# Kernel optimization log

Hardware: AMD Instinct MI355X
Metric: run time of the kernel (lower is better)

## Reference

```python
import jax, jax.numpy as jnp
import numpy as np

# Complete K-ary forest: B trees, depth D levels, BFS node numbering per tree.
B, K, D = 64, 4, 6
V, L = 600, 256
N_PER = (K ** D - 1) // (K - 1)   # 1365 nodes per tree
N = B * N_PER                      # 87360 total nodes


def _schedule():
    """Per-(depth, sibling_index) groups, mirroring the torch decode_train loop
    for a complete K-ary forest. Returns list of (d, s, node_idx, parent_idx)."""
    starts = [(K ** d - 1) // (K - 1) for d in range(D)]  # level offsets within a tree
    tree_off = np.arange(B)[:, None] * N_PER
    groups = []
    for d in range(D):
        for s in (range(1) if d == 0 else range(K)):
            if d == 0:
                p = np.arange(1)                      # root
                par = None
            else:
                p = np.arange(K ** (d - 1)) * K + s   # positions with sib_pos == s
                par = (tree_off + starts[d - 1] + (p // K)[None, :]).reshape(-1)
            idx = (tree_off + starts[d] + p[None, :]).reshape(-1)
            groups.append((d, s, jnp.asarray(idx),
                           None if par is None else jnp.asarray(par)))
    return groups

GROUPS = _schedule()


def _lstm(gx, h, c, W_hh, b_ih, b_hh):
    # torch LSTMCell, gate order i, f, g, o; gx = x @ W_ih^T precomputed.
    gates = gx + b_ih + h @ W_hh.T + b_hh
    i, f, g, o = jnp.split(gates, 4, axis=1)
    c_new = jax.nn.sigmoid(f) * c + jax.nn.sigmoid(i) * jnp.tanh(g)
    return jax.nn.sigmoid(o) * jnp.tanh(c_new), c_new


def setup_inputs() -> dict:
    key = jax.random.key(0)
    ks = jax.random.split(key, 20)
    w = lambda k, shape, s=0.05: jax.random.normal(k, shape, dtype=jnp.float32) * s
    return {
        'z': w(ks[0], (B, L), 1.0),
        'features': jax.random.randint(ks[1], (N,), 0, V),
        'W_ih_p': w(ks[2], (4 * L, V)), 'W_hh_p': w(ks[3], (4 * L, L)),
        'b_ih_p': w(ks[4], (4 * L,)), 'b_hh_p': w(ks[5], (4 * L,)),
        'W_ih_s': w(ks[6], (4 * L, V)), 'W_hh_s': w(ks[7], (4 * L, L)),
        'b_ih_s': w(ks[8], (4 * L,)), 'b_hh_s': w(ks[9], (4 * L,)),
        'U_parent': w(ks[10], (L, L)), 'U_sibling': w(ks[11], (L, L)),
        'W_label': w(ks[12], (V, L)), 'b_label': w(ks[13], (V,)),
        'W_depth': w(ks[14], (1, L)), 'b_depth': w(ks[15], (1,)),
        'W_width': w(ks[16], (1, L)), 'b_width': w(ks[17], (1,)),
        'w_off_p': w(ks[18], (1, 1), 1.0), 'w_off_s': w(ks[19], (1, 1), 1.0),
    }


def reference(z, features, W_ih_p, W_hh_p, b_ih_p, b_hh_p,
              W_ih_s, W_hh_s, b_ih_s, b_hh_s, U_parent, U_sibling,
              W_label, b_label, W_depth, b_depth, W_width, b_width,
              w_off_p, w_off_s):
    h_p = jnp.zeros((N, L), jnp.float32)
    c_p = jnp.zeros((N, L), jnp.float32)
    h_s = jnp.zeros((N, L), jnp.float32)
    c_s = jnp.zeros((N, L), jnp.float32)
    pred_labels = jnp.zeros((N, V), jnp.float32)
    pred_is_parent = jnp.zeros((N,), jnp.float32)
    pred_has_sib = jnp.zeros((N,), jnp.float32)

    for d, s, idx, pidx in GROUPS:
        G = idx.shape[0]
        if d == 0:
            h_par, c_par = z, jnp.zeros((B, L), jnp.float32)
        else:
            h_par, c_par = h_p[pidx], c_p[pidx]
        if s == 0:
            h_prev = jnp.zeros((G, L), jnp.float32)
            c_prev = jnp.zeros((G, L), jnp.float32)
        else:
            h_prev, c_prev = h_s[idx - 1], c_s[idx - 1]
        # group-constant teacher flags for a complete K-ary tree
        is_par = 1.0 if d < D - 1 else 0.0
        has_sib = 1.0 if (d > 0 and s < K - 1) else 0.0

        h_pred = jnp.tanh(h_par @ U_parent.T + h_prev @ U_sibling.T)
        logits = h_pred @ W_label.T + b_label
        p_par = jax.nn.sigmoid(h_pred @ W_depth.T + b_depth)[:, 0]
        p_sib = jax.nn.sigmoid(h_pred @ W_width.T + b_width)[:, 0]
        logp = jax.nn.log_softmax(
            logits + w_off_p[0, 0] * is_par + w_off_s[0, 0] * has_sib, axis=1)

        lab = features[idx]
        gx_p = jnp.take(W_ih_p, lab, axis=1).T  # one-hot @ W_ih^T as a gather
        gx_s = jnp.take(W_ih_s, lab, axis=1).T
        hp_new, cp_new = _lstm(gx_p, h_par, c_par, W_hh_p, b_ih_p, b_hh_p)
        hs_new, cs_new = _lstm(gx_s, h_prev, c_prev, W_hh_s, b_ih_s, b_hh_s)

        h_p = h_p.at[idx].set(hp_new)
        c_p = c_p.at[idx].set(cp_new)
        h_s = h_s.at[idx].set(hs_new)
        c_s = c_s.at[idx].set(cs_new)
        pred_labels = pred_labels.at[idx].set(logp)
        pred_is_parent = pred_is_parent.at[idx].set(p_par)
        pred_has_sib = pred_has_sib.at[idx].set(p_sib)

    # pack [N, V+2]: log-softmax labels, p(is_parent), p(has_sibling)
    return jnp.concatenate(
        [pred_labels, pred_is_parent[:, None], pred_has_sib[:, None]], axis=1)
```

## Files before the change

kernel.cpp:

```cpp
#include <hip/hip_runtime.h>


typedef unsigned short u16;
typedef short bf16x8 __attribute__((ext_vector_type(8)));
typedef float f32x4 __attribute__((ext_vector_type(4)));

#define NPER 1365
#define VDIM 600
#define VD2  602

__device__ __forceinline__ float b2f(u16 h) {
  union { unsigned u; float f; } v; v.u = ((unsigned)h) << 16; return v.f;
}
__device__ __forceinline__ u16 f2bf(float f) {
  union { float f; unsigned u; } v; v.f = f;
  unsigned r = v.u + 0x7fff + ((v.u >> 16) & 1);
  return (u16)(r >> 16);
}
__device__ __forceinline__ float fsigm(float x) {
  return __fdividef(1.f, 1.f + __expf(-x));
}
__device__ __forceinline__ float ftanh(float x) {
  float e = __expf(-2.f * fabsf(x));
  float r = __fdividef(1.f - e, 1.f + e);
  return x < 0.f ? -r : r;
}

__device__ __forceinline__ void ladder(int r, int& off, int& pcs, int& start) {
  if (r < 64)        { off = 0;    pcs = 0; start = 1;   }
  else if (r < 320)  { off = 64;   pcs = 2; start = 5;   }
  else if (r < 1344) { off = 320;  pcs = 4; start = 21;  }
  else if (r < 5440) { off = 1344; pcs = 6; start = 85;  }
  else               { off = 5440; pcs = 8; start = 341; }
}

__global__ void k_pack(
    const float* __restrict__ Upar, const float* __restrict__ Whhp,
    const float* __restrict__ Usib, const float* __restrict__ Whhs,
    const float* __restrict__ z, const float* __restrict__ Wihp,
    const float* __restrict__ Wihs, const float* __restrict__ Wlab,
    const float* __restrict__ Wd, const float* __restrict__ Ww,
    const float* __restrict__ blab, const float* __restrict__ bd,
    const float* __restrict__ bw, const float* __restrict__ bihp,
    const float* __restrict__ bhhp, const float* __restrict__ bihs,
    const float* __restrict__ bhhs,
    u16* __restrict__ UPWHHP, u16* __restrict__ USWHHS, u16* __restrict__ ZBF,
    u16* __restrict__ WIHPT, u16* __restrict__ WIHST, u16* __restrict__ WEXT,
    float* __restrict__ BE, float* __restrict__ BP, float* __restrict__ BS) {
  int i = blockIdx.x * 256 + threadIdx.x;
  if (i < 327680) {
    int r = i >> 8, c = i & 255;
    UPWHHP[i] = f2bf(r < 256 ? Upar[(r << 8) | c] : Whhp[((r - 256) << 8) | c]);
    return;
  }
  i -= 327680;
  if (i < 327680) {
    int r = i >> 8, c = i & 255;
    USWHHS[i] = f2bf(r < 256 ? Usib[(r << 8) | c] : Whhs[((r - 256) << 8) | c]);
    return;
  }
  i -= 327680;
  if (i < 16384) { ZBF[i] = f2bf(z[i]); return; }
  i -= 16384;
  if (i < 614400) {
    int r = i >> 10, c = i & 1023;
    WIHPT[i] = f2bf(Wihp[c * VDIM + r]); return;
  }
  i -= 614400;
  if (i < 614400) {
    int r = i >> 10, c = i & 1023;
    WIHST[i] = f2bf(Wihs[c * VDIM + r]); return;
  }
  i -= 614400;
  if (i < VD2 * 256) {
    int r = i >> 8, c = i & 255;
    float v = (r < VDIM) ? Wlab[r * 256 + c] : ((r == VDIM) ? Wd[c] : Ww[c]);
    WEXT[i] = f2bf(v); return;
  }
  i -= VD2 * 256;
  if (i < VD2) { BE[i] = (i < VDIM) ? blab[i] : ((i == VDIM) ? bd[0] : bw[0]); return; }
  i -= VD2;
  if (i < 1024) { BP[i] = bihp[i] + bhhp[i]; return; }
  i -= 1024;
  if (i < 1024) { BS[i] = bihs[i] + bhhs[i]; return; }
}

__global__ __launch_bounds__(256) void k_dual(
    const u16* __restrict__ A, const u16* __restrict__ B,
    u16* __restrict__ ppdst, int ppoff, float* __restrict__ uproj,
    u16* __restrict__ hroot, u16* __restrict__ gates, int M) {
  __shared__ __align__(16) u16 As[128 * 40];
  __shared__ __align__(16) u16 Bs[128 * 40];
  const int m0 = blockIdx.x * 128, n0 = blockIdx.y * 128;
  const int tid = threadIdx.x;
  const int wave = tid >> 6, lane = tid & 63;
  const int quad = lane >> 4, lr = lane & 15;
  const int wm = (wave >> 1) * 64, wn = (wave & 1) * 64;
  const int srow = tid >> 2;
  const int sch = (tid & 3) << 3;

  f32x4 acc[4][4] = {};
  for (int t = 0; t < 8; ++t) {
    const int kk = t * 32;
    bf16x8 a0 = *(const bf16x8*)(A + (size_t)(m0 + srow) * 256 + kk + sch);
    bf16x8 a1 = *(const bf16x8*)(A + (size_t)(m0 + srow + 64) * 256 + kk + sch);
    bf16x8 b0 = *(const bf16x8*)(B + (size_t)(n0 + srow) * 256 + kk + sch);
    bf16x8 b1 = *(const bf16x8*)(B + (size_t)(n0 + srow + 64) * 256 + kk + sch);
    __syncthreads();
    *(bf16x8*)&As[srow * 40 + sch] = a0;
    *(bf16x8*)&As[(srow + 64) * 40 + sch] = a1;
    *(bf16x8*)&Bs[srow * 40 + sch] = b0;
    *(bf16x8*)&Bs[(srow + 64) * 40 + sch] = b1;
    __syncthreads();
    bf16x8 af[4], bfr[4];
#pragma unroll
    for (int tm = 0; tm < 4; ++tm)
      af[tm] = *(const bf16x8*)&As[(wm + tm * 16 + lr) * 40 + quad * 8];
#pragma unroll
    for (int tn = 0; tn < 4; ++tn)
      bfr[tn] = *(const bf16x8*)&Bs[(wn + tn * 16 + lr) * 40 + quad * 8];
#pragma unroll
    for (int tm = 0; tm < 4; ++tm)
#pragma unroll
      for (int tn = 0; tn < 4; ++tn)
        acc[tm][tn] = __builtin_amdgcn_mfma_f32_16x16x32_bf16(
            af[tm], bfr[tn], acc[tm][tn], 0, 0, 0);
  }

  const bool isg = (n0 >= 256);
#pragma unroll
  for (int tn = 0; tn < 4; ++tn) {
    int col = n0 + wn + tn * 16 + lr;
#pragma unroll
    for (int tm = 0; tm < 4; ++tm) {
#pragma unroll
      for (int r = 0; r < 4; ++r) {
        int row = m0 + wm + tm * 16 + quad * 4 + r;
        if (row >= M) continue;
        float v = acc[tm][tn][r];
        if (isg) {
          gates[(size_t)row * 1024 + (col - 256)] = f2bf(v);
        } else if (hroot) {
          hroot[(size_t)row * NPER * 256 + col] = f2bf(ftanh(v));
        } else if (uproj) {
          uproj[(size_t)row * 256 + col] = v;
        } else {
          ppdst[(size_t)(ppoff + row) * 256 + col] = f2bf(v);
        }
      }
    }
  }
}


__global__ __launch_bounds__(256) void k_lstm_s0(
    const u16* __restrict__ wihT, const float* __restrict__ bias,
    const int* __restrict__ feat, u16* __restrict__ h, u16* __restrict__ c) {
  int r = blockIdx.x, u = threadIdx.x;
  int off, pcs, start; ladder(r, off, pcs, start);
  int lg = r - off;
  int t = lg >> pcs, j = lg & ((1 << pcs) - 1);
  int idx = t * NPER + start + 4 * j;
  int lab = feat[idx];
  const u16* wr = wihT + lab * 1024;
  float gi = b2f(wr[u])       + bias[u];
  float gg = b2f(wr[512 + u]) + bias[512 + u];
  float go = b2f(wr[768 + u]) + bias[768 + u];
  float cn = fsigm(gi) * ftanh(gg);
  float hn = fsigm(go) * ftanh(cn);
  h[(size_t)r * 256 + u] = f2bf(hn);
  c[(size_t)r * 256 + u] = f2bf(cn);
}

__global__ __launch_bounds__(256) void k_lstm_sibA(
    const u16* __restrict__ gates, const u16* __restrict__ wihT,
    const float* __restrict__ bias, const u16* __restrict__ c_in,
    const int* __restrict__ feat, u16* __restrict__ h, u16* __restrict__ c,
    int k) {
  int r = blockIdx.x, u = threadIdx.x;
  int off, pcs, start; ladder(r, off, pcs, start);
  int lg = r - off;
  int t = lg >> pcs, j = lg & ((1 << pcs) - 1);
  int idx = t * NPER + start + 4 * j + k;
  int lab = feat[idx];
  const u16* wr = wihT + lab * 1024;
  const u16* gr = gates + (size_t)r * 1024;
  float gi = b2f(wr[u])       + bias[u]       + b2f(gr[u]);
  float gf = b2f(wr[256 + u]) + bias[256 + u] + b2f(gr[256 + u]);
  float gg = b2f(wr[512 + u]) + bias[512 + u] + b2f(gr[512 + u]);
  float go = b2f(wr[768 + u]) + bias[768 + u] + b2f(gr[768 + u]);
  float cv = b2f(c_in[(size_t)r * 256 + u]);
  float cn = fsigm(gf) * cv + fsigm(gi) * ftanh(gg);
  float hn = fsigm(go) * ftanh(cn);
  h[(size_t)r * 256 + u] = f2bf(hn);
  c[(size_t)r * 256 + u] = f2bf(cn);
}

__global__ __launch_bounds__(256) void k_lstm_par(
    const u16* __restrict__ gates, const u16* __restrict__ wihT,
    const float* __restrict__ bias, const u16* __restrict__ c_in,
    const int* __restrict__ feat, u16* __restrict__ h, u16* __restrict__ c,
    int lsbits, int start) {
  int g = blockIdx.x, u = threadIdx.x;
  int t = g >> lsbits, p = g & ((1 << lsbits) - 1);
  int pr = lsbits ? ((t << (lsbits - 2)) | (p >> 2)) : g;
  int idx = t * NPER + start + p;
  int lab = feat[idx];
  const u16* wr = wihT + lab * 1024;
  const u16* gr = gates + (size_t)pr * 1024;
  float gi = b2f(wr[u])       + bias[u]       + b2f(gr[u]);
  float gf = b2f(wr[256 + u]) + bias[256 + u] + b2f(gr[256 + u]);
  float gg = b2f(wr[512 + u]) + bias[512 + u] + b2f(gr[512 + u]);
  float go = b2f(wr[768 + u]) + bias[768 + u] + b2f(gr[768 + u]);
  float cv = c_in ? b2f(c_in[(size_t)pr * 256 + u]) : 0.f;
  float cn = fsigm(gf) * cv + fsigm(gi) * ftanh(gg);
  float hn = fsigm(go) * ftanh(cn);
  h[(size_t)g * 256 + u] = f2bf(hn);
  c[(size_t)g * 256 + u] = f2bf(cn);
}

__global__ __launch_bounds__(256) void k_assemble(
    const u16* __restrict__ PPA, const float* __restrict__ U1,
    const float* __restrict__ U2, const float* __restrict__ U3,
    u16* __restrict__ HPRED) {
  int r = blockIdx.x, u = threadIdx.x;
  int off, pcs, start; ladder(r, off, pcs, start);
  int lg = r - off;
  int t = lg >> pcs, j = lg & ((1 << pcs) - 1);
  size_t base = ((size_t)(t * NPER + start + 4 * j)) * 256 + u;
  size_t ro = (size_t)r * 256 + u;
  float pp = b2f(PPA[ro]);
  HPRED[base]       = f2bf(ftanh(pp));
  HPRED[base + 256] = f2bf(ftanh(pp + U1[ro]));
  HPRED[base + 512] = f2bf(ftanh(pp + U2[ro]));
  HPRED[base + 768] = f2bf(ftanh(pp + U3[ro]));
}

__global__ __launch_bounds__(256, 2) void k_mm_tail(
    const u16* __restrict__ A, const u16* __restrict__ B,
    const float* __restrict__ bias, float* __restrict__ out) {
  __shared__ __align__(16) u16 As[32 * 264];
  __shared__ float smax[32][4], ssum[32][4], slz[32];
  const int m0 = blockIdx.x * 32;
  const int tid = threadIdx.x;
  const int wave = tid >> 6, lane = tid & 63;
  const int quad = lane >> 4, lr = lane & 15;
  const int c0 = wave * 160;

#pragma unroll
  for (int c = 0; c < 4; ++c) {
    int idx = c * 256 + tid;
    int row = idx >> 5, ch = (idx & 31) << 3;
    *(bf16x8*)&As[row * 264 + ch] =
        *(const bf16x8*)(A + (size_t)(m0 + row) * 256 + ch);
  }
  __syncthreads();

  f32x4 acc[2][10] = {};
#pragma unroll
  for (int t = 0; t < 8; ++t) {
    bf16x8 af[2], bfr[10];
#pragma unroll
    for (int tm = 0; tm < 2; ++tm)
      af[tm] = *(const bf16x8*)&As[(tm * 16 + lr) * 264 + t * 32 + quad * 8];
#pragma unroll
    for (int tn = 0; tn < 10; ++tn)
      bfr[tn] = *(const bf16x8*)(B + (size_t)(c0 + tn * 16 + lr) * 256 +
                                 t * 32 + quad * 8);
#pragma unroll
    for (int tm = 0; tm < 2; ++tm)
#pragma unroll
      for (int tn = 0; tn < 10; ++tn)
        acc[tm][tn] = __builtin_amdgcn_mfma_f32_16x16x32_bf16(
            af[tm], bfr[tn], acc[tm][tn], 0, 0, 0);
  }

  float bv[10]; bool val[10];
#pragma unroll
  for (int tn = 0; tn < 10; ++tn) {
    int col = c0 + tn * 16 + lr;
    val[tn] = (col < VDIM);
    bv[tn] = (col < VD2) ? bias[col] : 0.f;
  }

#pragma unroll
  for (int tm = 0; tm < 2; ++tm) {
#pragma unroll
    for (int r = 0; r < 4; ++r) {
      float mx = -1e30f;
#pragma unroll
      for (int tn = 0; tn < 10; ++tn)
        if (val[tn]) mx = fmaxf(mx, acc[tm][tn][r] + bv[tn]);
#pragma unroll
      for (int o = 1; o < 16; o <<= 1) mx = fmaxf(mx, __shfl_xor(mx, o, 64));
      if (lr == 0) smax[tm * 16 + quad * 4 + r][wave] = mx;
    }
  }
  __syncthreads();
#pragma unroll
  for (int tm = 0; tm < 2; ++tm) {
#pragma unroll
    for (int r = 0; r < 4; ++r) {
      int row = tm * 16 + quad * 4 + r;
      float fm = fmaxf(fmaxf(smax[row][0], smax[row][1]),
                       fmaxf(smax[row][2], smax[row][3]));
      float se = 0.f;
#pragma unroll
      for (int tn = 0; tn < 10; ++tn)
        if (val[tn]) se += __expf(acc[tm][tn][r] + bv[tn] - fm);
#pragma unroll
      for (int o = 1; o < 16; o <<= 1) se += __shfl_xor(se, o, 64);
      if (lr == 0) ssum[row][wave] = se;
    }
  }
  __syncthreads();
  if (tid < 32) {
    float fm = fmaxf(fmaxf(smax[tid][0], smax[tid][1]),
                     fmaxf(smax[tid][2], smax[tid][3]));
    slz[tid] = fm + __logf(ssum[tid][0] + ssum[tid][1] +
                           ssum[tid][2] + ssum[tid][3]);
  }
  __syncthreads();

#pragma unroll
  for (int tm = 0; tm < 2; ++tm) {
#pragma unroll
    for (int tn = 0; tn < 10; ++tn) {
      int col = c0 + tn * 16 + lr;
      if (col >= VD2) continue;
#pragma unroll
      for (int r = 0; r < 4; ++r) {
        int row = tm * 16 + quad * 4 + r;
        float v = acc[tm][tn][r] + bv[tn];
        out[(size_t)(m0 + row) * VD2 + col] =
            (col < VDIM) ? (v - slz[row]) : fsigm(v);
      }
    }
  }
}


extern "C" void kernel_launch(void* const* d_in, const int* in_sizes, int n_in,
                              void* d_out, int out_size, void* d_ws, size_t ws_size,
                              hipStream_t stream) {
  const float* z    = (const float*)d_in[0];
  const int*   feat = (const int*)d_in[1];
  const float* Wihp = (const float*)d_in[2];
  const float* Whhp = (const float*)d_in[3];
  const float* bihp = (const float*)d_in[4];
  const float* bhhp = (const float*)d_in[5];
  const float* Wihs = (const float*)d_in[6];
  const float* Whhs = (const float*)d_in[7];
  const float* bihs = (const float*)d_in[8];
  const float* bhhs = (const float*)d_in[9];
  const float* Upar = (const float*)d_in[10];
  const float* Usib = (const float*)d_in[11];
  const float* Wlab = (const float*)d_in[12];
  const float* blab = (const float*)d_in[13];
  const float* Wd   = (const float*)d_in[14];
  const float* bd   = (const float*)d_in[15];
  const float* Ww   = (const float*)d_in[16];
  const float* bw   = (const float*)d_in[17];
  float* out = (float*)d_out;

  char* w = (char*)d_ws;
  auto alloc = [&](size_t bytes) {
    char* p = w; w += (bytes + 255) & ~(size_t)255; return p;
  };
  u16*   UPWHHP = (u16*)alloc((size_t)1280 * 256 * 2);
  u16*   USWHHS = (u16*)alloc((size_t)1280 * 256 * 2);
  u16*   ZBF    = (u16*)alloc((size_t)128 * 256 * 2);
  u16*   WIHPT  = (u16*)alloc((size_t)VDIM * 1024 * 2);
  u16*   WIHST  = (u16*)alloc((size_t)VDIM * 1024 * 2);
  u16*   WEXT   = (u16*)alloc((size_t)640 * 256 * 2);
  float* BE     = (float*)alloc(VD2 * 4);
  float* BP     = (float*)alloc(1024 * 4);
  float* BS     = (float*)alloc(1024 * 4);
  const size_t CR = 21888;
  u16*   HSA[3], *CSA[3];
  for (int k = 0; k < 3; ++k) {
    HSA[k] = (u16*)alloc(CR * 256 * 2);
    CSA[k] = (u16*)alloc(CR * 256 * 2);
  }
  float* UPROJ[3];
  for (int k = 0; k < 3; ++k) UPROJ[k] = (float*)alloc(CR * 256 * 4);
  u16*   PPA   = (u16*)alloc(CR * 256 * 2);
  const size_t SB = (size_t)16384 * 256 * 2;
  u16* HP[2] = {(u16*)alloc(SB), (u16*)alloc(SB)};
  u16* CP[2] = {(u16*)alloc(SB), (u16*)alloc(SB)};
  u16*   GATES  = (u16*)alloc(CR * 1024 * 2);
  u16*   GATESP = (u16*)alloc((size_t)4096 * 1024 * 2);
  u16*   HPRED  = (u16*)alloc((size_t)87424 * 256 * 2);

  const int ppoff[6] = {0, 0, 64, 320, 1344, 5440};

  k_pack<<<8037, 256, 0, stream>>>(Upar, Whhp, Usib, Whhs, z, Wihp, Wihs,
                                   Wlab, Wd, Ww, blab, bd, bw, bihp, bhhp,
                                   bihs, bhhs, UPWHHP, USWHHS, ZBF, WIHPT,
                                   WIHST, WEXT, BE, BP, BS);
  k_lstm_s0<<<21824, 256, 0, stream>>>(WIHST, BS, feat, HSA[0], CSA[0]);

  k_dual<<<dim3(171, 10), 256, 0, stream>>>(HSA[0], USWHHS, nullptr, 0,
                                            UPROJ[0], nullptr, GATES, 21824);
  k_lstm_sibA<<<21824, 256, 0, stream>>>(GATES, WIHST, BS, CSA[0], feat,
                                         HSA[1], CSA[1], 1);
  k_dual<<<dim3(171, 10), 256, 0, stream>>>(HSA[1], USWHHS, nullptr, 0,
                                            UPROJ[1], nullptr, GATES, 21824);
  k_lstm_sibA<<<21824, 256, 0, stream>>>(GATES, WIHST, BS, CSA[1], feat,
                                         HSA[2], CSA[2], 2);
  k_dual<<<dim3(171, 2), 256, 0, stream>>>(HSA[2], USWHHS, nullptr, 0,
                                           UPROJ[2], nullptr, nullptr, 21824);

  k_dual<<<dim3(1, 10), 256, 0, stream>>>(ZBF, UPWHHP, nullptr, 0, nullptr,
                                          HPRED, GATESP, 64);
  k_lstm_par<<<64, 256, 0, stream>>>(GATESP, WIHPT, BP, nullptr, feat,
                                     HP[0], CP[0], 0, 0);
  const int starts[6] = {0, 1, 5, 21, 85, 341};
  int cur = 0;
  for (int d = 0; d < 4; ++d) {
    const int M = 64 << (2 * d);
    k_dual<<<dim3((M + 127) / 128, 10), 256, 0, stream>>>(
        HP[cur], UPWHHP, PPA, ppoff[d + 1], nullptr, nullptr, GATESP, M);
    k_lstm_par<<<64 << (2 * (d + 1)), 256, 0, stream>>>(
        GATESP, WIHPT, BP, CP[cur], feat, HP[1 - cur], CP[1 - cur],
        2 * (d + 1), starts[d + 1]);
    cur = 1 - cur;
  }
  k_dual<<<dim3(128, 2), 256, 0, stream>>>(HP[cur], UPWHHP, PPA, ppoff[5],
                                           nullptr, nullptr, nullptr, 16384);

  k_assemble<<<21824, 256, 0, stream>>>(PPA, UPROJ[0], UPROJ[1], UPROJ[2],
                                        HPRED);
  k_mm_tail<<<2730, 256, 0, stream>>>(HPRED, WEXT, BE, out);

  (void)in_sizes; (void)n_in; (void)out_size; (void)ws_size;
}
```

Baseline: 650.9 us.

## Co-schedule independent sibling and parent chains in fused launches, fold assemble into GEMM epilogue

Merges the independent sibling-chain and parent-chain kernels into combined launches that split work by block index. This cuts the launch count and lets small parent-level GEMMs and LSTMs overlap with the large sibling work. The assemble step for deeper levels moves into the parent GEMM epilogue, which shrinks the PPA buffer and removes a read/write pass. Output and UPROJ stores become nontemporal. Fused kernels pay for the largest shared-memory and register footprint of any branch, and the modes add some branching.

After: 863.2 us. 1.33x slower.

```diff
diff --git a/kernel.cpp b/kernel.cpp
--- a/kernel.cpp
+++ b/kernel.cpp
@@ -8,6 +8,11 @@
 #define NPER 1365
 #define VDIM 600
 #define VD2  602
+
+#define MODE_PPA   0
+#define MODE_UPROJ 1
+#define MODE_ROOT  2
+#define MODE_EPI   3
 
 __device__ __forceinline__ float b2f(u16 h) {
   union { unsigned u; float f; } v; v.u = ((unsigned)h) << 16; return v.f;
@@ -85,13 +90,16 @@
   if (i < 1024) { BS[i] = bihs[i] + bhhs[i]; return; }
 }
 
-__global__ __launch_bounds__(256) void k_dual(
-    const u16* __restrict__ A, const u16* __restrict__ B,
-    u16* __restrict__ ppdst, int ppoff, float* __restrict__ uproj,
-    u16* __restrict__ hroot, u16* __restrict__ gates, int M) {
-  __shared__ __align__(16) u16 As[128 * 40];
-  __shared__ __align__(16) u16 Bs[128 * 40];
-  const int m0 = blockIdx.x * 128, n0 = blockIdx.y * 128;
+__device__ __forceinline__ void dev_dual(
+    int tile, int nx, const u16* __restrict__ A, const u16* __restrict__ B,
+    int M, int mode, u16* __restrict__ ppa, int ppoff,
+    float* __restrict__ uproj, u16* __restrict__ gates,
+    u16* __restrict__ hpred, const float* __restrict__ U1,
+    const float* __restrict__ U2, const float* __restrict__ U3,
+    int lsb, int startd) {
+  static __shared__ __align__(16) u16 As[128 * 40];
+  static __shared__ __align__(16) u16 Bs[128 * 40];
+  const int m0 = (tile % nx) * 128, n0 = (tile / nx) * 128;
   const int tid = threadIdx.x;
   const int wave = tid >> 6, lane = tid & 63;
   const int quad = lane >> 4, lr = lane & 15;
@@ -140,12 +148,20 @@
         float v = acc[tm][tn][r];
         if (isg) {
           gates[(size_t)row * 1024 + (col - 256)] = f2bf(v);
-        } else if (hroot) {
-          hroot[(size_t)row * NPER * 256 + col] = f2bf(ftanh(v));
-        } else if (uproj) {
-          uproj[(size_t)row * 256 + col] = v;
+        } else if (mode == MODE_PPA) {
+          ppa[(size_t)(ppoff + row) * 256 + col] = f2bf(v);
+        } else if (mode == MODE_UPROJ) {
+          __builtin_nontemporal_store(v, &uproj[(size_t)row * 256 + col]);
+        } else if (mode == MODE_ROOT) {
+          hpred[(size_t)row * NPER * 256 + col] = f2bf(ftanh(v));
         } else {
-          ppdst[(size_t)(ppoff + row) * 256 + col] = f2bf(v);
+          int t2 = row >> lsb, j = row & ((1 << lsb) - 1);
+          size_t bb = ((size_t)(t2 * NPER + startd + 4 * j)) * 256 + col;
+          size_t ro = (size_t)(ppoff + row) * 256 + col;
+          hpred[bb]       = f2bf(ftanh(v));
+          hpred[bb + 256] = f2bf(ftanh(v + U1[ro]));
+          hpred[bb + 512] = f2bf(ftanh(v + U2[ro]));
+          hpred[bb + 768] = f2bf(ftanh(v + U3[ro]));
         }
       }
     }
@@ -153,15 +169,14 @@
 }
 
 
-__global__ __launch_bounds__(256) void k_lstm_s0(
-    const u16* __restrict__ wihT, const float* __restrict__ bias,
-    const int* __restrict__ feat, u16* __restrict__ h, u16* __restrict__ c) {
-  int r = blockIdx.x, u = threadIdx.x;
+__device__ __forceinline__ void dev_s0(int r, const u16* __restrict__ wihT,
+    const float* __restrict__ bias, const int* __restrict__ feat,
+    u16* __restrict__ h, u16* __restrict__ c) {
+  int u = threadIdx.x;
   int off, pcs, start; ladder(r, off, pcs, start);
   int lg = r - off;
   int t = lg >> pcs, j = lg & ((1 << pcs) - 1);
-  int idx = t * NPER + start + 4 * j;
-  int lab = feat[idx];
+  int lab = feat[t * NPER + start + 4 * j];
   const u16* wr = wihT + lab * 1024;
   float gi = b2f(wr[u])       + bias[u];
   float gg = b2f(wr[512 + u]) + bias[512 + u];
@@ -172,17 +187,15 @@
   c[(size_t)r * 256 + u] = f2bf(cn);
 }
 
-__global__ __launch_bounds__(256) void k_lstm_sibA(
+__device__ __forceinline__ void dev_lstm_sib(int r, int k,
     const u16* __restrict__ gates, const u16* __restrict__ wihT,
     const float* __restrict__ bias, const u16* __restrict__ c_in,
-    const int* __restrict__ feat, u16* __restrict__ h, u16* __restrict__ c,
-    int k) {
-  int r = blockIdx.x, u = threadIdx.x;
+    const int* __restrict__ feat, u16* __restrict__ h, u16* __restrict__ c) {
+  int u = threadIdx.x;
   int off, pcs, start; ladder(r, off, pcs, start);
   int lg = r - off;
   int t = lg >> pcs, j = lg & ((1 << pcs) - 1);
-  int idx = t * NPER + start + 4 * j + k;
-  int lab = feat[idx];
+  int lab = feat[t * NPER + start + 4 * j + k];
   const u16* wr = wihT + lab * 1024;
   const u16* gr = gates + (size_t)r * 1024;
   float gi = b2f(wr[u])       + bias[u]       + b2f(gr[u]);
@@ -196,16 +209,15 @@
   c[(size_t)r * 256 + u] = f2bf(cn);
 }
 
-__global__ __launch_bounds__(256) void k_lstm_par(
+__device__ __forceinline__ void dev_lstm_par(int g,
     const u16* __restrict__ gates, const u16* __restrict__ wihT,
     const float* __restrict__ bias, const u16* __restrict__ c_in,
     const int* __restrict__ feat, u16* __restrict__ h, u16* __restrict__ c,
     int lsbits, int start) {
-  int g = blockIdx.x, u = threadIdx.x;
+  int u = threadIdx.x;
   int t = g >> lsbits, p = g & ((1 << lsbits) - 1);
   int pr = lsbits ? ((t << (lsbits - 2)) | (p >> 2)) : g;
-  int idx = t * NPER + start + p;
-  int lab = feat[idx];
+  int lab = feat[t * NPER + start + p];
   const u16* wr = wihT + lab * 1024;
   const u16* gr = gates + (size_t)pr * 1024;
   float gi = b2f(wr[u])       + bias[u]       + b2f(gr[u]);
@@ -219,11 +231,11 @@
   c[(size_t)g * 256 + u] = f2bf(cn);
 }
 
-__global__ __launch_bounds__(256) void k_assemble(
+__device__ __forceinline__ void dev_assemble(int r,
     const u16* __restrict__ PPA, const float* __restrict__ U1,
     const float* __restrict__ U2, const float* __restrict__ U3,
     u16* __restrict__ HPRED) {
-  int r = blockIdx.x, u = threadIdx.x;
+  int u = threadIdx.x;
   int off, pcs, start; ladder(r, off, pcs, start);
   int lg = r - off;
   int t = lg >> pcs, j = lg & ((1 << pcs) - 1);
@@ -236,6 +248,72 @@
   HPRED[base + 768] = f2bf(ftanh(pp + U3[ro]));
 }
 
+
+__global__ __launch_bounds__(256) void k_s0_zdual(
+    const u16* WIHST, const float* BS, const int* feat, u16* h, u16* c,
+    const u16* ZBF, const u16* UPWHHP, u16* HPRED, u16* GATESP) {
+  int b = blockIdx.x;
+  if (b < 21824)
+    dev_s0(b, WIHST, BS, feat, h, c);
+  else
+    dev_dual(b - 21824, 1, ZBF, UPWHHP, 64, MODE_ROOT, nullptr, 0, nullptr,
+             GATESP, HPRED, nullptr, nullptr, nullptr, 0, 0);
+}
+
+__global__ __launch_bounds__(256) void k_sibdual_plstm(
+    int nSib, int nx, const u16* HSAin, const u16* USWHHS,
+    float* UPROJk, u16* GATES,
+    const u16* GATESP, const u16* WIHPT, const float* BP, const u16* CPin,
+    const int* feat, u16* HPout, u16* CPout, int lsbits, int startp) {
+  int b = blockIdx.x;
+  if (b < nSib)
+    dev_dual(b, nx, HSAin, USWHHS, 21824, MODE_UPROJ, nullptr, 0, UPROJk,
+             GATES, nullptr, nullptr, nullptr, nullptr, 0, 0);
+  else
+    dev_lstm_par(b - nSib, GATESP, WIHPT, BP, CPin, feat, HPout, CPout,
+                 lsbits, startp);
+}
+
+__global__ __launch_bounds__(256) void k_siblstm_pdual(
+    int kSib, const u16* GATES, const u16* WIHST, const float* BS,
+    const u16* CSAin, const int* feat, u16* HSAout, u16* CSAout,
+    int nx, const u16* HPin, const u16* UPWHHP, int Mpar,
+    u16* PPA, int ppoff, u16* GATESP) {
+  int b = blockIdx.x;
+  if (b < 21824)
+    dev_lstm_sib(b, kSib, GATES, WIHST, BS, CSAin, feat, HSAout, CSAout);
+  else
+    dev_dual(b - 21824, nx, HPin, UPWHHP, Mpar, MODE_PPA, PPA, ppoff, nullptr,
+             GATESP, nullptr, nullptr, nullptr, nullptr, 0, 0);
+}
+
+__global__ __launch_bounds__(256) void k_pdual_epi(
+    int nx, const u16* HPin, const u16* UPWHHP, int M, u16* GATESP,
+    u16* HPRED, const float* U1, const float* U2, const float* U3,
+    int ppoff, int lsb, int startd) {
+  dev_dual(blockIdx.x, nx, HPin, UPWHHP, M, MODE_EPI, nullptr, ppoff, nullptr,
+           GATESP, HPRED, U1, U2, U3, lsb, startd);
+}
+
+__global__ __launch_bounds__(256) void k_plstm_asm(
+    const u16* GATESP, const u16* WIHPT, const float* BP, const u16* CPin,
+    const int* feat, u16* HPout, u16* CPout,
+    const u16* PPA, const float* U1, const float* U2, const float* U3,
+    u16* HPRED) {
+  int b = blockIdx.x;
+  if (b < 4096)
+    dev_lstm_par(b, GATESP, WIHPT, BP, CPin, feat, HPout, CPout, 6, 21);
+  else
+    dev_assemble(b - 4096, PPA, U1, U2, U3, HPRED);
+}
+
+__global__ __launch_bounds__(256) void k_plstm(
+    const u16* GATESP, const u16* WIHPT, const float* BP, const u16* CPin,
+    const int* feat, u16* HPout, u16* CPout, int lsbits, int start) {
+  dev_lstm_par(blockIdx.x, GATESP, WIHPT, BP, CPin, feat, HPout, CPout,
+               lsbits, start);
+}
+
 __global__ __launch_bounds__(256, 2) void k_mm_tail(
     const u16* __restrict__ A, const u16* __restrict__ B,
     const float* __restrict__ bias, float* __restrict__ out) {
@@ -332,8 +410,8 @@
       for (int r = 0; r < 4; ++r) {
         int row = tm * 16 + quad * 4 + r;
         float v = acc[tm][tn][r] + bv[tn];
-        out[(size_t)(m0 + row) * VD2 + col] =
-            (col < VDIM) ? (v - slz[row]) : fsigm(v);
+        float o = (col < VDIM) ? (v - slz[row]) : fsigm(v);
+        __builtin_nontemporal_store(o, &out[(size_t)(m0 + row) * VD2 + col]);
       }
     }
   }
@@ -384,7 +462,7 @@
   }
   float* UPROJ[3];
   for (int k = 0; k < 3; ++k) UPROJ[k] = (float*)alloc(CR * 256 * 4);
-  u16*   PPA   = (u16*)alloc(CR * 256 * 2);
+  u16*   PPA   = (u16*)alloc((size_t)384 * 256 * 2);
   const size_t SB = (size_t)16384 * 256 * 2;
   u16* HP[2] = {(u16*)alloc(SB), (u16*)alloc(SB)};
   u16* CP[2] = {(u16*)alloc(SB), (u16*)alloc(SB)};
@@ -392,45 +470,41 @@
   u16*   GATESP = (u16*)alloc((size_t)4096 * 1024 * 2);
   u16*   HPRED  = (u16*)alloc((size_t)87424 * 256 * 2);
 
-  const int ppoff[6] = {0, 0, 64, 320, 1344, 5440};
-
   k_pack<<<8037, 256, 0, stream>>>(Upar, Whhp, Usib, Whhs, z, Wihp, Wihs,
                                    Wlab, Wd, Ww, blab, bd, bw, bihp, bhhp,
                                    bihs, bhhs, UPWHHP, USWHHS, ZBF, WIHPT,
                                    WIHST, WEXT, BE, BP, BS);
-  k_lstm_s0<<<21824, 256, 0, stream>>>(WIHST, BS, feat, HSA[0], CSA[0]);
-
-  k_dual<<<dim3(171, 10), 256, 0, stream>>>(HSA[0], USWHHS, nullptr, 0,
-                                            UPROJ[0], nullptr, GATES, 21824);
-  k_lstm_sibA<<<21824, 256, 0, stream>>>(GATES, WIHST, BS, CSA[0], feat,
-                                         HSA[1], CSA[1], 1);
-  k_dual<<<dim3(171, 10), 256, 0, stream>>>(HSA[1], USWHHS, nullptr, 0,
-                                            UPROJ[1], nullptr, GATES, 21824);
-  k_lstm_sibA<<<21824, 256, 0, stream>>>(GATES, WIHST, BS, CSA[1], feat,
-                                         HSA[2], CSA[2], 2);
-  k_dual<<<dim3(171, 2), 256, 0, stream>>>(HSA[2], USWHHS, nullptr, 0,
-                                           UPROJ[2], nullptr, nullptr, 21824);
-
-  k_dual<<<dim3(1, 10), 256, 0, stream>>>(ZBF, UPWHHP, nullptr, 0, nullptr,
-                                          HPRED, GATESP, 64);
-  k_lstm_par<<<64, 256, 0, stream>>>(GATESP, WIHPT, BP, nullptr, feat,
-                                     HP[0], CP[0], 0, 0);
-  const int starts[6] = {0, 1, 5, 21, 85, 341};
-  int cur = 0;
-  for (int d = 0; d < 4; ++d) {
-    const int M = 64 << (2 * d);
-    k_dual<<<dim3((M + 127) / 128, 10), 256, 0, stream>>>(
-        HP[cur], UPWHHP, PPA, ppoff[d + 1], nullptr, nullptr, GATESP, M);
-    k_lstm_par<<<64 << (2 * (d + 1)), 256, 0, stream>>>(
-        GATESP, WIHPT, BP, CP[cur], feat, HP[1 - cur], CP[1 - cur],
-        2 * (d + 1), starts[d + 1]);
-    cur = 1 - cur;
-  }
-  k_dual<<<dim3(128, 2), 256, 0, stream>>>(HP[cur], UPWHHP, PPA, ppoff[5],
-                                           nullptr, nullptr, nullptr, 16384);
-
-  k_assemble<<<21824, 256, 0, stream>>>(PPA, UPROJ[0], UPROJ[1], UPROJ[2],
-                                        HPRED);
+  k_s0_zdual<<<21834, 256, 0, stream>>>(WIHST, BS, feat, HSA[0], CSA[0],
+                                        ZBF, UPWHHP, HPRED, GATESP);
+  k_sibdual_plstm<<<1710 + 64, 256, 0, stream>>>(
+      1710, 171, HSA[0], USWHHS, UPROJ[0], GATES,
+      GATESP, WIHPT, BP, nullptr, feat, HP[0], CP[0], 0, 0);
+  k_siblstm_pdual<<<21824 + 10, 256, 0, stream>>>(
+      1, GATES, WIHST, BS, CSA[0], feat, HSA[1], CSA[1],
+      1, HP[0], UPWHHP, 64, PPA, 0, GATESP);
+  k_sibdual_plstm<<<1710 + 256, 256, 0, stream>>>(
+      1710, 171, HSA[1], USWHHS, UPROJ[1], GATES,
+      GATESP, WIHPT, BP, CP[0], feat, HP[1], CP[1], 2, 1);
+  k_siblstm_pdual<<<21824 + 20, 256, 0, stream>>>(
+      2, GATES, WIHST, BS, CSA[1], feat, HSA[2], CSA[2],
+      2, HP[1], UPWHHP, 256, PPA, 64, GATESP);
+  k_sibdual_plstm<<<342 + 1024, 256, 0, stream>>>(
+      342, 171, HSA[2], USWHHS, UPROJ[2], nullptr,
+      GATESP, WIHPT, BP, CP[1], feat, HP[0], CP[0], 4, 5);
+  k_pdual_epi<<<80, 256, 0, stream>>>(8, HP[0], UPWHHP, 1024, GATESP,
+                                      HPRED, UPROJ[0], UPROJ[1], UPROJ[2],
+                                      320, 4, 21);
+  k_plstm_asm<<<4096 + 320, 256, 0, stream>>>(
+      GATESP, WIHPT, BP, CP[0], feat, HP[1], CP[1],
+      PPA, UPROJ[0], UPROJ[1], UPROJ[2], HPRED);
+  k_pdual_epi<<<320, 256, 0, stream>>>(32, HP[1], UPWHHP, 4096, GATESP,
+                                       HPRED, UPROJ[0], UPROJ[1], UPROJ[2],
+                                       1344, 6, 85);
+  k_plstm<<<16384, 256, 0, stream>>>(GATESP, WIHPT, BP, CP[1], feat,
+                                     HP[0], CP[0], 8, 85);
+  k_pdual_epi<<<256, 256, 0, stream>>>(128, HP[0], UPWHHP, 16384, nullptr,
+                                       HPRED, UPROJ[0], UPROJ[1], UPROJ[2],
+                                       5440, 8, 341);
   k_mm_tail<<<2730, 256, 0, stream>>>(HPRED, WEXT, BE, out);
 
   (void)in_sizes; (void)n_in; (void)out_size; (void)ws_size;
```

## Co-schedule parent and sibling chains in merged launches and fuse assemble into tail

Applied to the files above, without the earlier changes.

The independent parent-LSTM and sibling-LSTM chains now share grids: their GEMM tiles are combined in one k_gg launch and their elementwise LSTM steps in one k_ll launch, cutting launch count and letting the small parent-level work overlap with the large sibling work. The k_assemble pass and the HPRED buffer are removed. The tail kernel now builds h_pred tiles on the fly from PPA and UPROJ with tanh, and the root rows come from a separate HROOT buffer. The tail tile also shrinks from 32 to 16 rows with a higher occupancy bound. The trade-off is that B weights are reloaded twice as often in the tail, and the tail's load path now has more divergent indexing.

Measured after the change: 727.2 us. +11.7%, slower.

```diff
diff --git a/kernel.cpp b/kernel.cpp
--- a/kernel.cpp
+++ b/kernel.cpp
@@ -8,6 +8,10 @@
 #define NPER 1365
 #define VDIM 600
 #define VD2  602
+
+#define MODE_PPA   0
+#define MODE_UPROJ 1
+#define MODE_ROOT  2
 
 __device__ __forceinline__ float b2f(u16 h) {
   union { unsigned u; float f; } v; v.u = ((unsigned)h) << 16; return v.f;
@@ -85,13 +89,14 @@
   if (i < 1024) { BS[i] = bihs[i] + bhhs[i]; return; }
 }
 
-__global__ __launch_bounds__(256) void k_dual(
-    const u16* __restrict__ A, const u16* __restrict__ B,
-    u16* __restrict__ ppdst, int ppoff, float* __restrict__ uproj,
-    u16* __restrict__ hroot, u16* __restrict__ gates, int M) {
-  __shared__ __align__(16) u16 As[128 * 40];
-  __shared__ __align__(16) u16 Bs[128 * 40];
-  const int m0 = blockIdx.x * 128, n0 = blockIdx.y * 128;
+__device__ __forceinline__ void dev_dual(
+    int tile, int nx, const u16* __restrict__ A, const u16* __restrict__ B,
+    int M, int mode, u16* __restrict__ ppa, int ppoff,
+    float* __restrict__ uproj, u16* __restrict__ gates,
+    u16* __restrict__ hroot) {
+  static __shared__ __align__(16) u16 As[128 * 40];
+  static __shared__ __align__(16) u16 Bs[128 * 40];
+  const int m0 = (tile % nx) * 128, n0 = (tile / nx) * 128;
   const int tid = threadIdx.x;
   const int wave = tid >> 6, lane = tid & 63;
   const int quad = lane >> 4, lr = lane & 15;
@@ -140,12 +145,12 @@
         float v = acc[tm][tn][r];
         if (isg) {
           gates[(size_t)row * 1024 + (col - 256)] = f2bf(v);
-        } else if (hroot) {
-          hroot[(size_t)row * NPER * 256 + col] = f2bf(ftanh(v));
-        } else if (uproj) {
+        } else if (mode == MODE_PPA) {
+          ppa[(size_t)(ppoff + row) * 256 + col] = f2bf(v);
+        } else if (mode == MODE_UPROJ) {
           uproj[(size_t)row * 256 + col] = v;
         } else {
-          ppdst[(size_t)(ppoff + row) * 256 + col] = f2bf(v);
+          hroot[(size_t)row * 256 + col] = f2bf(ftanh(v));
         }
       }
     }
@@ -153,15 +158,14 @@
 }
 
 
-__global__ __launch_bounds__(256) void k_lstm_s0(
-    const u16* __restrict__ wihT, const float* __restrict__ bias,
-    const int* __restrict__ feat, u16* __restrict__ h, u16* __restrict__ c) {
-  int r = blockIdx.x, u = threadIdx.x;
+__device__ __forceinline__ void dev_s0(int r, const u16* __restrict__ wihT,
+    const float* __restrict__ bias, const int* __restrict__ feat,
+    u16* __restrict__ h, u16* __restrict__ c) {
+  int u = threadIdx.x;
   int off, pcs, start; ladder(r, off, pcs, start);
   int lg = r - off;
   int t = lg >> pcs, j = lg & ((1 << pcs) - 1);
-  int idx = t * NPER + start + 4 * j;
-  int lab = feat[idx];
+  int lab = feat[t * NPER + start + 4 * j];
   const u16* wr = wihT + lab * 1024;
   float gi = b2f(wr[u])       + bias[u];
   float gg = b2f(wr[512 + u]) + bias[512 + u];
@@ -172,17 +176,15 @@
   c[(size_t)r * 256 + u] = f2bf(cn);
 }
 
-__global__ __launch_bounds__(256) void k_lstm_sibA(
+__device__ __forceinline__ void dev_lstm_sib(int r, int k,
     const u16* __restrict__ gates, const u16* __restrict__ wihT,
     const float* __restrict__ bias, const u16* __restrict__ c_in,
-    const int* __restrict__ feat, u16* __restrict__ h, u16* __restrict__ c,
-    int k) {
-  int r = blockIdx.x, u = threadIdx.x;
+    const int* __restrict__ feat, u16* __restrict__ h, u16* __restrict__ c) {
+  int u = threadIdx.x;
   int off, pcs, start; ladder(r, off, pcs, start);
   int lg = r - off;
   int t = lg >> pcs, j = lg & ((1 << pcs) - 1);
-  int idx = t * NPER + start + 4 * j + k;
-  int lab = feat[idx];
+  int lab = feat[t * NPER + start + 4 * j + k];
   const u16* wr = wihT + lab * 1024;
   const u16* gr = gates + (size_t)r * 1024;
   float gi = b2f(wr[u])       + bias[u]       + b2f(gr[u]);
@@ -196,16 +198,15 @@
   c[(size_t)r * 256 + u] = f2bf(cn);
 }
 
-__global__ __launch_bounds__(256) void k_lstm_par(
+__device__ __forceinline__ void dev_lstm_par(int g,
     const u16* __restrict__ gates, const u16* __restrict__ wihT,
     const float* __restrict__ bias, const u16* __restrict__ c_in,
     const int* __restrict__ feat, u16* __restrict__ h, u16* __restrict__ c,
     int lsbits, int start) {
-  int g = blockIdx.x, u = threadIdx.x;
+  int u = threadIdx.x;
   int t = g >> lsbits, p = g & ((1 << lsbits) - 1);
   int pr = lsbits ? ((t << (lsbits - 2)) | (p >> 2)) : g;
-  int idx = t * NPER + start + p;
-  int lab = feat[idx];
+  int lab = feat[t * NPER + start + p];
   const u16* wr = wihT + lab * 1024;
   const u16* gr = gates + (size_t)pr * 1024;
   float gi = b2f(wr[u])       + bias[u]       + b2f(gr[u]);
@@ -219,60 +220,113 @@
   c[(size_t)g * 256 + u] = f2bf(cn);
 }
 
-__global__ __launch_bounds__(256) void k_assemble(
-    const u16* __restrict__ PPA, const float* __restrict__ U1,
-    const float* __restrict__ U2, const float* __restrict__ U3,
-    u16* __restrict__ HPRED) {
-  int r = blockIdx.x, u = threadIdx.x;
-  int off, pcs, start; ladder(r, off, pcs, start);
-  int lg = r - off;
-  int t = lg >> pcs, j = lg & ((1 << pcs) - 1);
-  size_t base = ((size_t)(t * NPER + start + 4 * j)) * 256 + u;
-  size_t ro = (size_t)r * 256 + u;
-  float pp = b2f(PPA[ro]);
-  HPRED[base]       = f2bf(ftanh(pp));
-  HPRED[base + 256] = f2bf(ftanh(pp + U1[ro]));
-  HPRED[base + 512] = f2bf(ftanh(pp + U2[ro]));
-  HPRED[base + 768] = f2bf(ftanh(pp + U3[ro]));
-}
-
-__global__ __launch_bounds__(256, 2) void k_mm_tail(
-    const u16* __restrict__ A, const u16* __restrict__ B,
+
+__global__ __launch_bounds__(256) void k_s0(
+    const u16* WIHST, const float* BS, const int* feat, u16* h, u16* c) {
+  dev_s0(blockIdx.x, WIHST, BS, feat, h, c);
+}
+
+__global__ __launch_bounds__(256) void k_gg(
+    int nA,
+    const u16* Aa, const u16* Ba, int Ma, int nxa, int modea,
+    u16* ppaa, int ppoffa, float* uproja, u16* gatesa, u16* hroota,
+    const u16* Ab, const u16* Bb, int Mb, int nxb, int modeb,
+    u16* ppab, int ppoffb, float* uprojb, u16* gatesb, u16* hrootb) {
+  int b = blockIdx.x;
+  if (b < nA)
+    dev_dual(b, nxa, Aa, Ba, Ma, modea, ppaa, ppoffa, uproja, gatesa, hroota);
+  else
+    dev_dual(b - nA, nxb, Ab, Bb, Mb, modeb, ppab, ppoffb, uprojb, gatesb,
+             hrootb);
+}
+
+__global__ __launch_bounds__(256) void k_gemm(
+    const u16* A, const u16* B, int M, int nx, int mode,
+    u16* ppa, int ppoff, float* uproj, u16* gates, u16* hroot) {
+  dev_dual(blockIdx.x, nx, A, B, M, mode, ppa, ppoff, uproj, gates, hroot);
+}
+
+__global__ __launch_bounds__(256) void k_ll(
+    int nP,
+    const u16* gatesP, const u16* WIHPT, const float* BP, const u16* cpin,
+    u16* hpout, u16* cpout, int lsbits, int startp,
+    int kS, const u16* gatesS, const u16* WIHST, const float* BS,
+    const u16* csin, u16* hsout, u16* csout, const int* feat) {
+  int b = blockIdx.x;
+  if (b < nP)
+    dev_lstm_par(b, gatesP, WIHPT, BP, cpin, feat, hpout, cpout, lsbits,
+                 startp);
+  else
+    dev_lstm_sib(b - nP, kS, gatesS, WIHST, BS, csin, feat, hsout, csout);
+}
+
+__global__ __launch_bounds__(256) void k_plstm(
+    const u16* gatesP, const u16* WIHPT, const float* BP, const u16* cpin,
+    const int* feat, u16* hpout, u16* cpout, int lsbits, int start) {
+  dev_lstm_par(blockIdx.x, gatesP, WIHPT, BP, cpin, feat, hpout, cpout,
+               lsbits, start);
+}
+
+__global__ __launch_bounds__(256, 4) void k_tail16(
+    const u16* __restrict__ HROOT, const u16* __restrict__ PPA,
+    const float* __restrict__ U1, const float* __restrict__ U2,
+    const float* __restrict__ U3, const u16* __restrict__ B,
     const float* __restrict__ bias, float* __restrict__ out) {
-  __shared__ __align__(16) u16 As[32 * 264];
-  __shared__ float smax[32][4], ssum[32][4], slz[32];
-  const int m0 = blockIdx.x * 32;
+  __shared__ __align__(16) u16 As[16 * 264];
+  __shared__ float smax[16][4], ssum[16][4], slz[16];
+  const int m0 = blockIdx.x * 16;
   const int tid = threadIdx.x;
   const int wave = tid >> 6, lane = tid & 63;
   const int quad = lane >> 4, lr = lane & 15;
   const int c0 = wave * 160;
 
 #pragma unroll
-  for (int c = 0; c < 4; ++c) {
-    int idx = c * 256 + tid;
+  for (int cch = 0; cch < 2; ++cch) {
+    int idx = cch * 256 + tid;
     int row = idx >> 5, ch = (idx & 31) << 3;
-    *(bf16x8*)&As[row * 264 + ch] =
-        *(const bf16x8*)(A + (size_t)(m0 + row) * 256 + ch);
+    int node = m0 + row;
+    int t = node / NPER;
+    int q = node - t * NPER;
+    bf16x8 v8;
+    if (q == 0) {
+      v8 = *(const bf16x8*)(HROOT + (size_t)t * 256 + ch);
+    } else {
+      int off, pcs, start;
+      if (q < 5)        { off = 0;    pcs = 0; start = 1;   }
+      else if (q < 21)  { off = 64;   pcs = 2; start = 5;   }
+      else if (q < 85)  { off = 320;  pcs = 4; start = 21;  }
+      else if (q < 341) { off = 1344; pcs = 6; start = 85;  }
+      else              { off = 5440; pcs = 8; start = 341; }
+      int qq = q - start;
+      int s = qq & 3, j = qq >> 2;
+      int r = off + (t << pcs) + j;
+      size_t ro = (size_t)r * 256 + ch;
+      bf16x8 pp = *(const bf16x8*)(PPA + ro);
+      const float* Us = (s == 1) ? U1 : ((s == 2) ? U2 : U3);
+#pragma unroll
+      for (int e = 0; e < 8; ++e) {
+        float v = b2f((u16)pp[e]);
+        if (s) v += Us[ro + e];
+        v8[e] = (short)f2bf(ftanh(v));
+      }
+    }
+    *(bf16x8*)&As[row * 264 + ch] = v8;
   }
   __syncthreads();
 
-  f32x4 acc[2][10] = {};
+  f32x4 acc[10] = {};
 #pragma unroll
   for (int t = 0; t < 8; ++t) {
-    bf16x8 af[2], bfr[10];
-#pragma unroll
-    for (int tm = 0; tm < 2; ++tm)
-      af[tm] = *(const bf16x8*)&As[(tm * 16 + lr) * 264 + t * 32 + quad * 8];
+    bf16x8 af = *(const bf16x8*)&As[lr * 264 + t * 32 + quad * 8];
+    bf16x8 bfr[10];
 #pragma unroll
     for (int tn = 0; tn < 10; ++tn)
       bfr[tn] = *(const bf16x8*)(B + (size_t)(c0 + tn * 16 + lr) * 256 +
                                  t * 32 + quad * 8);
 #pragma unroll
-    for (int tm = 0; tm < 2; ++tm)
-#pragma unroll
-      for (int tn = 0; tn < 10; ++tn)
-        acc[tm][tn] = __builtin_amdgcn_mfma_f32_16x16x32_bf16(
-            af[tm], bfr[tn], acc[tm][tn], 0, 0, 0);
+    for (int tn = 0; tn < 10; ++tn)
+      acc[tn] = __builtin_amdgcn_mfma_f32_16x16x32_bf16(af, bfr[tn], acc[tn],
+                                                        0, 0, 0);
   }
 
   float bv[10]; bool val[10];
@@ -284,37 +338,31 @@
   }
 
 #pragma unroll
-  for (int tm = 0; tm < 2; ++tm) {
-#pragma unroll
-    for (int r = 0; r < 4; ++r) {
-      float mx = -1e30f;
-#pragma unroll
-      for (int tn = 0; tn < 10; ++tn)
-        if (val[tn]) mx = fmaxf(mx, acc[tm][tn][r] + bv[tn]);
-#pragma unroll
-      for (int o = 1; o < 16; o <<= 1) mx = fmaxf(mx, __shfl_xor(mx, o, 64));
-      if (lr == 0) smax[tm * 16 + quad * 4 + r][wave] = mx;
-    }
+  for (int r = 0; r < 4; ++r) {
+    float mx = -1e30f;
+#pragma unroll
+    for (int tn = 0; tn < 10; ++tn)
+      if (val[tn]) mx = fmaxf(mx, acc[tn][r] + bv[tn]);
+#pragma unroll
+    for (int o = 1; o < 16; o <<= 1) mx = fmaxf(mx, __shfl_xor(mx, o, 64));
+    if (lr == 0) smax[quad * 4 + r][wave] = mx;
   }
   __syncthreads();
 #pragma unroll
-  for (int tm = 0; tm < 2; ++tm) {
-#pragma unroll
-    for (int r = 0; r < 4; ++r) {
-      int row = tm * 16 + quad * 4 + r;
-      float fm = fmaxf(fmaxf(smax[row][0], smax[row][1]),
-                       fmaxf(smax[row][2], smax[row][3]));
-      float se = 0.f;
-#pragma unroll
-      for (int tn = 0; tn < 10; ++tn)
-        if (val[tn]) se += __expf(acc[tm][tn][r] + bv[tn] - fm);
-#pragma unroll
-      for (int o = 1; o < 16; o <<= 1) se += __shfl_xor(se, o, 64);
-      if (lr == 0) ssum[row][wave] = se;
-    }
+  for (int r = 0; r < 4; ++r) {
+    int row = quad * 4 + r;
+    float fm = fmaxf(fmaxf(smax[row][0], smax[row][1]),
+                     fmaxf(smax[row][2], smax[row][3]));
+    float se = 0.f;
+#pragma unroll
+    for (int tn = 0; tn < 10; ++tn)
+      if (val[tn]) se += __expf(acc[tn][r] + bv[tn] - fm);
+#pragma unroll
+    for (int o = 1; o < 16; o <<= 1) se += __shfl_xor(se, o, 64);
+    if (lr == 0) ssum[row][wave] = se;
   }
   __syncthreads();
-  if (tid < 32) {
+  if (tid < 16) {
     float fm = fmaxf(fmaxf(smax[tid][0], smax[tid][1]),
                      fmaxf(smax[tid][2], smax[tid][3]));
     slz[tid] = fm + __logf(ssum[tid][0] + ssum[tid][1] +
@@ -323,18 +371,15 @@
   __syncthreads();
 
 #pragma unroll
-  for (int tm = 0; tm < 2; ++tm) {
-#pragma unroll
-    for (int tn = 0; tn < 10; ++tn) {
-      int col = c0 + tn * 16 + lr;
-      if (col >= VD2) continue;
-#pragma unroll
-      for (int r = 0; r < 4; ++r) {
-        int row = tm * 16 + quad * 4 + r;
-        float v = acc[tm][tn][r] + bv[tn];
-        out[(size_t)(m0 + row) * VD2 + col] =
-            (col < VDIM) ? (v - slz[row]) : fsigm(v);
-      }
+  for (int tn = 0; tn < 10; ++tn) {
+    int col = c0 + tn * 16 + lr;
+    if (col >= VD2) continue;
+#pragma unroll
+    for (int r = 0; r < 4; ++r) {
+      int row = quad * 4 + r;
+      float v = acc[tn][r] + bv[tn];
+      out[(size_t)(m0 + row) * VD2 + col] =
+          (col < VDIM) ? (v - slz[row]) : fsigm(v);
     }
   }
 }
@@ -385,53 +430,53 @@
   float* UPROJ[3];
   for (int k = 0; k < 3; ++k) UPROJ[k] = (float*)alloc(CR * 256 * 4);
   u16*   PPA   = (u16*)alloc(CR * 256 * 2);
+  u16*   HROOT = (u16*)alloc((size_t)64 * 256 * 2);
   const size_t SB = (size_t)16384 * 256 * 2;
   u16* HP[2] = {(u16*)alloc(SB), (u16*)alloc(SB)};
   u16* CP[2] = {(u16*)alloc(SB), (u16*)alloc(SB)};
   u16*   GATES  = (u16*)alloc(CR * 1024 * 2);
   u16*   GATESP = (u16*)alloc((size_t)4096 * 1024 * 2);
-  u16*   HPRED  = (u16*)alloc((size_t)87424 * 256 * 2);
-
-  const int ppoff[6] = {0, 0, 64, 320, 1344, 5440};
 
   k_pack<<<8037, 256, 0, stream>>>(Upar, Whhp, Usib, Whhs, z, Wihp, Wihs,
                                    Wlab, Wd, Ww, blab, bd, bw, bihp, bhhp,
                                    bihs, bhhs, UPWHHP, USWHHS, ZBF, WIHPT,
                                    WIHST, WEXT, BE, BP, BS);
-  k_lstm_s0<<<21824, 256, 0, stream>>>(WIHST, BS, feat, HSA[0], CSA[0]);
-
-  k_dual<<<dim3(171, 10), 256, 0, stream>>>(HSA[0], USWHHS, nullptr, 0,
-                                            UPROJ[0], nullptr, GATES, 21824);
-  k_lstm_sibA<<<21824, 256, 0, stream>>>(GATES, WIHST, BS, CSA[0], feat,
-                                         HSA[1], CSA[1], 1);
-  k_dual<<<dim3(171, 10), 256, 0, stream>>>(HSA[1], USWHHS, nullptr, 0,
-                                            UPROJ[1], nullptr, GATES, 21824);
-  k_lstm_sibA<<<21824, 256, 0, stream>>>(GATES, WIHST, BS, CSA[1], feat,
-                                         HSA[2], CSA[2], 2);
-  k_dual<<<dim3(171, 2), 256, 0, stream>>>(HSA[2], USWHHS, nullptr, 0,
-                                           UPROJ[2], nullptr, nullptr, 21824);
-
-  k_dual<<<dim3(1, 10), 256, 0, stream>>>(ZBF, UPWHHP, nullptr, 0, nullptr,
-                                          HPRED, GATESP, 64);
-  k_lstm_par<<<64, 256, 0, stream>>>(GATESP, WIHPT, BP, nullptr, feat,
-                                     HP[0], CP[0], 0, 0);
-  const int starts[6] = {0, 1, 5, 21, 85, 341};
-  int cur = 0;
-  for (int d = 0; d < 4; ++d) {
-    const int M = 64 << (2 * d);
-    k_dual<<<dim3((M + 127) / 128, 10), 256, 0, stream>>>(
-        HP[cur], UPWHHP, PPA, ppoff[d + 1], nullptr, nullptr, GATESP, M);
-    k_lstm_par<<<64 << (2 * (d + 1)), 256, 0, stream>>>(
-        GATESP, WIHPT, BP, CP[cur], feat, HP[1 - cur], CP[1 - cur],
-        2 * (d + 1), starts[d + 1]);
-    cur = 1 - cur;
-  }
-  k_dual<<<dim3(128, 2), 256, 0, stream>>>(HP[cur], UPWHHP, PPA, ppoff[5],
-                                           nullptr, nullptr, nullptr, 16384);
-
-  k_assemble<<<21824, 256, 0, stream>>>(PPA, UPROJ[0], UPROJ[1], UPROJ[2],
-                                        HPRED);
-  k_mm_tail<<<2730, 256, 0, stream>>>(HPRED, WEXT, BE, out);
+  k_s0<<<21824, 256, 0, stream>>>(WIHST, BS, feat, HSA[0], CSA[0]);
+  k_gg<<<10 + 1710, 256, 0, stream>>>(
+      10,
+      ZBF, UPWHHP, 64, 1, MODE_ROOT, nullptr, 0, nullptr, GATESP, HROOT,
+      HSA[0], USWHHS, 21824, 171, MODE_UPROJ, nullptr, 0, UPROJ[0], GATES,
+      nullptr);
+  k_ll<<<64 + 21824, 256, 0, stream>>>(
+      64, GATESP, WIHPT, BP, nullptr, HP[0], CP[0], 0, 0,
+      1, GATES, WIHST, BS, CSA[0], HSA[1], CSA[1], feat);
+  k_gg<<<10 + 1710, 256, 0, stream>>>(
+      10,
+      HP[0], UPWHHP, 64, 1, MODE_PPA, PPA, 0, nullptr, GATESP, nullptr,
+      HSA[1], USWHHS, 21824, 171, MODE_UPROJ, nullptr, 0, UPROJ[1], GATES,
+      nullptr);
+  k_ll<<<256 + 21824, 256, 0, stream>>>(
+      256, GATESP, WIHPT, BP, CP[0], HP[1], CP[1], 2, 1,
+      2, GATES, WIHST, BS, CSA[1], HSA[2], CSA[2], feat);
+  k_gg<<<20 + 342, 256, 0, stream>>>(
+      20,
+      HP[1], UPWHHP, 256, 2, MODE_PPA, PPA, 64, nullptr, GATESP, nullptr,
+      HSA[2], USWHHS, 21824, 171, MODE_UPROJ, nullptr, 0, UPROJ[2], nullptr,
+      nullptr);
+  k_plstm<<<1024, 256, 0, stream>>>(GATESP, WIHPT, BP, CP[1], feat,
+                                    HP[0], CP[0], 4, 5);
+  k_gemm<<<80, 256, 0, stream>>>(HP[0], UPWHHP, 1024, 8, MODE_PPA,
+                                 PPA, 320, nullptr, GATESP, nullptr);
+  k_plstm<<<4096, 256, 0, stream>>>(GATESP, WIHPT, BP, CP[0], feat,
+                                    HP[1], CP[1], 6, 21);
+  k_gemm<<<320, 256, 0, stream>>>(HP[1], UPWHHP, 4096, 32, MODE_PPA,
+                                  PPA, 1344, nullptr, GATESP, nullptr);
+  k_plstm<<<16384, 256, 0, stream>>>(GATESP, WIHPT, BP, CP[1], feat,
+                                     HP[0], CP[0], 8, 85);
+  k_gemm<<<256, 256, 0, stream>>>(HP[0], UPWHHP, 16384, 128, MODE_PPA,
+                                  PPA, 5440, nullptr, nullptr, nullptr);
+  k_tail16<<<5460, 256, 0, stream>>>(HROOT, PPA, UPROJ[0], UPROJ[1], UPROJ[2],
+                                     WEXT, BE, out);
 
   (void)in_sizes; (void)n_in; (void)out_size; (void)ws_size;
 }
```
